# Kernel tuning notes

Hardware: AMD Instinct MI355X
Metric: run time of the kernel (lower is better)

The kernel has to match this reference:

```python
import jax, jax.numpy as jnp
import numpy as np

IN_F, OUT_F = 256, 256
GRID, ORDER = 5, 3
K = GRID + ORDER + 1  # 9 knots
EPS_MINMAX = 1e-7     # K.epsilon()
EPS_BN = 1e-3         # keras BatchNormalization default epsilon


def setup_inputs() -> dict:
    key = jax.random.key(0)
    ks = jax.random.split(key, 4)
    x = jax.random.normal(ks[0], (32, 32, 32, IN_F), dtype=jnp.float32)
    he = lambda k, shape, fan_in: jax.random.normal(k, shape, jnp.float32) * np.sqrt(2.0 / fan_in)
    base_weight = he(ks[1], (IN_F, OUT_F), IN_F)
    spline_weight = he(ks[2], (OUT_F, IN_F, K), IN_F * K)
    spline_scaler = jnp.ones((OUT_F, IN_F), jnp.float32)
    return {
        'x': x,
        'base_weight': base_weight,
        'spline_weight': spline_weight,
        'spline_scaler': spline_scaler,
        'bn_base_gamma': jnp.ones((OUT_F,), jnp.float32),
        'bn_base_beta': jnp.zeros((OUT_F,), jnp.float32),
        'bn_base_mean': jnp.zeros((OUT_F,), jnp.float32),
        'bn_base_var': jnp.ones((OUT_F,), jnp.float32),
        'bn_spline_gamma': jnp.ones((OUT_F,), jnp.float32),
        'bn_spline_beta': jnp.zeros((OUT_F,), jnp.float32),
        'bn_spline_mean': jnp.zeros((OUT_F,), jnp.float32),
        'bn_spline_var': jnp.ones((OUT_F,), jnp.float32),
    }


def _bn(z, gamma, beta, mean, var):
    # Keras BatchNormalization, inference mode (training=False)
    return gamma * (z - mean) * jax.lax.rsqrt(var + EPS_BN) + beta


def reference(x, base_weight, spline_weight, spline_scaler,
              bn_base_gamma, bn_base_beta, bn_base_mean, bn_base_var,
              bn_spline_gamma, bn_spline_beta, bn_spline_mean, bn_spline_var):
    B, H, W, _ = x.shape
    xf = x.reshape(-1, IN_F)  # [N, in]

    # base path: GEMM -> BN -> SiLU
    base = xf @ base_weight
    base = jax.nn.silu(_bn(base, bn_base_gamma, bn_base_beta, bn_base_mean, bn_base_var))

    # min-max normalize per feature over the flattened batch
    x_min = jnp.min(xf, axis=0, keepdims=True)
    x_max = jnp.max(xf, axis=0, keepdims=True)
    xn = (xf - x_min) / (x_max - x_min + EPS_MINMAX)

    # triangle basis: relu(1 - |x - knot|), knots = linspace(-1, 1, K)
    knots = jnp.linspace(-1.0, 1.0, K, dtype=jnp.float32)
    basis = jnp.maximum(0.0, 1.0 - jnp.abs(xn[:, :, None] - knots[None, None, :]))  # [N, in, K]

    # scaled spline weight, flattened GEMM
    w = (spline_weight * spline_scaler[:, :, None]).reshape(OUT_F, IN_F * K)  # [out, in*K]
    spline = basis.reshape(-1, IN_F * K) @ w.T  # [N, out]
    spline = _bn(spline, bn_spline_gamma, bn_spline_beta, bn_spline_mean, bn_spline_var)

    out = base + spline
    return out.reshape(B, H, W, OUT_F)
```

## Files before the change

kernel.cpp:

```cpp
#include <hip/hip_runtime.h>
#include <stdint.h>
#include <stddef.h>

typedef _Float16 h2 __attribute__((ext_vector_type(2)));
typedef _Float16 h8 __attribute__((ext_vector_type(8)));
typedef float f4 __attribute__((ext_vector_type(4)));

union Hfrag { h2 p[4]; h8 v; };

#define WS_PMIN   0
#define WS_PMAX   524288
#define WS_BT     0
#define WS_SMALL  1048576
#define WS_SCALEV (WS_SMALL + 0)
#define WS_BKN    (WS_SMALL + 1024)
#define WS_C0     (WS_SMALL + 3072)
#define WS_BSC    (WS_SMALL + 4096)
#define WS_BSH    (WS_SMALL + 5120)
#define WS_SSC    (WS_SMALL + 6144)
#define WS_SSH    (WS_SMALL + 7168)

__global__ __launch_bounds__(256) void kan_minmax(const float* __restrict__ x,
                                                  float* __restrict__ pmin,
                                                  float* __restrict__ pmax) {
  __shared__ f4 smn[4][64], smx[4][64];
  const int b = blockIdx.x, t = threadIdx.x;
  const int fq = t & 63, rg = t >> 6;
  const float* p = x + (size_t)b * 64 * 256 + (size_t)rg * 16 * 256 + fq * 4;
  f4 mn = (f4)(3.402823466e38f), mx = (f4)(-3.402823466e38f);
#pragma unroll
  for (int j = 0; j < 16; ++j) {
    f4 v = *(const f4*)(p + (size_t)j * 256);
    mn = __builtin_elementwise_min(mn, v);
    mx = __builtin_elementwise_max(mx, v);
  }
  smn[rg][fq] = mn; smx[rg][fq] = mx;
  __syncthreads();
  if (rg == 0) {
#pragma unroll
    for (int g = 1; g < 4; ++g) {
      mn = __builtin_elementwise_min(mn, smn[g][fq]);
      mx = __builtin_elementwise_max(mx, smx[g][fq]);
    }
    *(f4*)(pmin + (size_t)b * 256 + fq * 4) = mn;
    *(f4*)(pmax + (size_t)b * 256 + fq * 4) = mx;
  }
}

__global__ __launch_bounds__(256) void kan_finalize(
    const float* __restrict__ pmin, const float* __restrict__ pmax,
    const float* __restrict__ g1, const float* __restrict__ b1,
    const float* __restrict__ m1, const float* __restrict__ v1,
    const float* __restrict__ g2, const float* __restrict__ b2,
    const float* __restrict__ m2, const float* __restrict__ v2,
    float* __restrict__ scalev, _Float16* __restrict__ bkn,
    float* __restrict__ bscv, float* __restrict__ bshv,
    float* __restrict__ sscv, float* __restrict__ sshv) {
  __shared__ float smn[4][64], smx[4][64];
  const int t = threadIdx.x;
  const int ol = t & 63, pg = t >> 6;
  const int o = blockIdx.x * 64 + ol;
  float mn = 3.402823466e38f, mx = -3.402823466e38f;
  for (int p = pg * 128; p < pg * 128 + 128; ++p) {
    mn = fminf(mn, pmin[(size_t)p * 256 + o]);
    mx = fmaxf(mx, pmax[(size_t)p * 256 + o]);
  }
  smn[pg][ol] = mn; smx[pg][ol] = mx;
  __syncthreads();
  if (pg == 0) {
#pragma unroll
    for (int g = 1; g < 4; ++g) {
      mn = fminf(mn, smn[g][ol]);
      mx = fmaxf(mx, smx[g][ol]);
    }
    const float rng = mx - mn + 1e-7f;
    scalev[o] = 1.0f / rng;
    const float step = 0.25f * rng;
#pragma unroll
    for (int j = 0; j < 4; ++j)
      bkn[j * 256 + o] = (_Float16)(mn + step * (float)j);
    const float bs = g1[o] / sqrtf(v1[o] + 1e-3f);
    bscv[o] = bs;
    bshv[o] = b1[o] - m1[o] * bs;
    const float ss = g2[o] / sqrtf(v2[o] + 1e-3f);
    sscv[o] = ss;
    sshv[o] = b2[o] - m2[o] * ss;
  }
}

__global__ __launch_bounds__(256) void kan_buildw(
    const float* __restrict__ spline_w, const float* __restrict__ spline_s,
    const float* __restrict__ base_w, const float* __restrict__ scalev,
    _Float16* __restrict__ Bt, float* __restrict__ C0) {
  const int og = blockIdx.x;
  const int i  = threadIdx.x;
  const float* wp = spline_w + (size_t)(og * 256 + i) * 9;
  const float w1 = wp[1], w2 = wp[2], w3 = wp[3], w4 = wp[4];
  const float w5 = wp[5], w6 = wp[6], w7 = wp[7], w8 = wp[8];
  const float s  = spline_s[og * 256 + i];
  const float sc = scalev[i];
  const float wp0 = 0.25f*w1 + 0.5f*w2 + 0.75f*w3 + w4 + 0.75f*w5 + 0.5f*w6 + 0.25f*w7;
  float wj[4];
  wj[0] = (w5 + w6 + w7 + w8) - (w1 + w2 + w3 + w4);
  wj[1] = w1 - 2.0f * w5;
  wj[2] = w2 - 2.0f * w6;
  wj[3] = w3 - 2.0f * w7;
  const float ssc = s * sc;
  const int half = og >> 7, o = og & 127, ic = i >> 5, kk = i & 31;
#pragma unroll
  for (int j = 0; j < 4; ++j) {
    const int ks = j * 8 + ic;
    Bt[((size_t)(ks * 2 + half) * 128 + o) * 32 + kk] = (_Float16)(wj[j] * ssc);
  }
  Bt[((size_t)((32 + ic) * 2 + half) * 128 + o) * 32 + kk] =
      (_Float16)base_w[(size_t)i * 256 + og];
  __shared__ float red[256];
  red[i] = wp0 * s;
  __syncthreads();
  for (int st = 128; st > 0; st >>= 1) {
    if (i < st) red[i] += red[i + st];
    __syncthreads();
  }
  if (i == 0) C0[og] = red[0];
}

__global__ __launch_bounds__(256, 2) void kan_gemm(
    const float* __restrict__ x, const _Float16* __restrict__ Bt,
    const _Float16* __restrict__ bkn, const float* __restrict__ C0,
    const float* __restrict__ bscv, const float* __restrict__ bshv,
    const float* __restrict__ sscv, const float* __restrict__ sshv,
    float* __restrict__ out) {
  const int tid = threadIdx.x;
  const int lane = tid & 63;
  const int wv = tid >> 6;
  const int wm = wv >> 1, wn = wv & 1;
  const int lr = lane & 15, lg = lane >> 4;
  const int mt = blockIdx.x & 255, nt = blockIdx.x >> 8;

  const int rowA = mt * 128 + wm * 64 + lr;
  const int colB = wn * 64 + lr;

  f4 accS[4][4], accB[4][4];
#pragma unroll
  for (int m = 0; m < 4; ++m)
#pragma unroll
    for (int n = 0; n < 4; ++n) { accS[m][n] = (f4)0.0f; accB[m][n] = (f4)0.0f; }

  const char* btbase = (const char*)Bt + (size_t)nt * 8192 + (size_t)colB * 64 + (size_t)lg * 16;

  h2 hz; hz[0] = (_Float16)0.0f; hz[1] = (_Float16)0.0f;

  f4 xa[4], xb[4];
  {
    const int ib = lg * 8;
#pragma unroll
    for (int m = 0; m < 4; ++m) {
      const float* px = x + (size_t)(rowA + m * 16) * 256 + ib;
      xa[m] = *(const f4*)px; xb[m] = *(const f4*)(px + 4);
    }
  }

#pragma unroll 1
  for (int ic = 0; ic < 8; ++ic) {
    Hfrag bb[4];
#pragma unroll
    for (int j = 0; j < 4; ++j)
      bb[j].v = *(const h8*)(bkn + j * 256 + ic * 32 + lg * 8);

    Hfrag xh[4];
#pragma unroll
    for (int m = 0; m < 4; ++m) {
      xh[m].p[0][0] = (_Float16)xa[m].x; xh[m].p[0][1] = (_Float16)xa[m].y;
      xh[m].p[1][0] = (_Float16)xa[m].z; xh[m].p[1][1] = (_Float16)xa[m].w;
      xh[m].p[2][0] = (_Float16)xb[m].x; xh[m].p[2][1] = (_Float16)xb[m].y;
      xh[m].p[3][0] = (_Float16)xb[m].z; xh[m].p[3][1] = (_Float16)xb[m].w;
    }

    if (ic < 7) {
      const int ib = (ic + 1) * 32 + lg * 8;
#pragma unroll
      for (int m = 0; m < 4; ++m) {
        const float* px = x + (size_t)(rowA + m * 16) * 256 + ib;
        xa[m] = *(const f4*)px; xb[m] = *(const f4*)(px + 4);
      }
    }

    const char* bpic = btbase + (size_t)ic * 16384;

#pragma unroll
    for (int it = 0; it < 4; ++it) {
      Hfrag bf[4];
#pragma unroll
      for (int n = 0; n < 4; ++n)
        bf[n].v = *(const h8*)(bpic + (size_t)it * 131072 + n * 1024);
      Hfrag af[4];
#pragma unroll
      for (int m = 0; m < 4; ++m)
#pragma unroll
        for (int q = 0; q < 4; ++q) {
          h2 d = xh[m].p[q] - bb[it].p[q];
          af[m].p[q] = __builtin_elementwise_max(d, hz);
        }
#pragma unroll
      for (int m = 0; m < 4; ++m)
#pragma unroll
        for (int n = 0; n < 4; ++n)
          accS[m][n] = __builtin_amdgcn_mfma_f32_16x16x32_f16(af[m].v, bf[n].v, accS[m][n], 0, 0, 0);
    }

    {
      Hfrag bf[4];
#pragma unroll
      for (int n = 0; n < 4; ++n)
        bf[n].v = *(const h8*)(bpic + 524288 + n * 1024);
#pragma unroll
      for (int m = 0; m < 4; ++m)
#pragma unroll
        for (int n = 0; n < 4; ++n)
          accB[m][n] = __builtin_amdgcn_mfma_f32_16x16x32_f16(xh[m].v, bf[n].v, accB[m][n], 0, 0, 0);
    }
  }

#pragma unroll
  for (int n = 0; n < 4; ++n) {
    const int col = nt * 128 + colB + n * 16;
    const float vbs = bscv[col], vbh = bshv[col];
    const float vss = sscv[col];
    const float vsh = sshv[col] + vss * C0[col];
#pragma unroll
    for (int m = 0; m < 4; ++m) {
      const int row0 = mt * 128 + wm * 64 + m * 16 + lg * 4;
#pragma unroll
      for (int r = 0; r < 4; ++r) {
        const float zb = accB[m][n][r] * vbs + vbh;
        const float si = zb / (1.0f + __expf(-zb));
        const float val = si + accS[m][n][r] * vss + vsh;
        out[(size_t)(row0 + r) * 256 + col] = val;
      }
    }
  }
}

extern "C" void kernel_launch(void* const* d_in, const int* in_sizes, int n_in,
                              void* d_out, int out_size, void* d_ws, size_t ws_size,
                              hipStream_t stream) {
  const float* x        = (const float*)d_in[0];
  const float* base_w   = (const float*)d_in[1];
  const float* spline_w = (const float*)d_in[2];
  const float* spline_s = (const float*)d_in[3];
  const float* g1 = (const float*)d_in[4];
  const float* b1 = (const float*)d_in[5];
  const float* m1 = (const float*)d_in[6];
  const float* v1 = (const float*)d_in[7];
  const float* g2 = (const float*)d_in[8];
  const float* b2 = (const float*)d_in[9];
  const float* m2 = (const float*)d_in[10];
  const float* v2 = (const float*)d_in[11];
  float* out = (float*)d_out;
  char* ws = (char*)d_ws;

  float* pmin     = (float*)(ws + WS_PMIN);
  float* pmax     = (float*)(ws + WS_PMAX);
  _Float16* Bt    = (_Float16*)(ws + WS_BT);
  float* scalev   = (float*)(ws + WS_SCALEV);
  _Float16* bkn   = (_Float16*)(ws + WS_BKN);
  float* C0       = (float*)(ws + WS_C0);
  float* bscv     = (float*)(ws + WS_BSC);
  float* bshv     = (float*)(ws + WS_BSH);
  float* sscv     = (float*)(ws + WS_SSC);
  float* sshv     = (float*)(ws + WS_SSH);

  kan_minmax<<<512, 256, 0, stream>>>(x, pmin, pmax);
  kan_finalize<<<4, 256, 0, stream>>>(pmin, pmax, g1, b1, m1, v1, g2, b2, m2, v2,
                                      scalev, bkn, bscv, bshv, sscv, sshv);
  kan_buildw<<<256, 256, 0, stream>>>(spline_w, spline_s, base_w, scalev, Bt, C0);
  kan_gemm<<<512, 256, 0, stream>>>(x, Bt, bkn, C0, bscv, bshv, sscv, sshv, out);
}
```

Measured before the change: 155.0 us.

## Parallelize min/max finalize over 64 blocks and double-buffer B fragments in GEMM

The finalize kernel now runs as 64 blocks that each reduce 4 features across all 512 partials with vector loads and a shared-memory tree, replacing 4 blocks that looped serially over partials. In the GEMM main loop, B fragments are double-buffered so the next spline tile's loads are issued before the current tile's MFMAs. Knot fragments are loaded per step instead of all at once, and the prefetch of the next x chunk moves behind a sched_barrier. The aim is to cut the serial latency of the small finalize kernel and hide global-load latency in the GEMM, at the cost of more live registers.

```diff
diff --git a/kernel.cpp b/kernel.cpp
--- a/kernel.cpp
+++ b/kernel.cpp
@@ -56,35 +56,40 @@
     float* __restrict__ scalev, _Float16* __restrict__ bkn,
     float* __restrict__ bscv, float* __restrict__ bshv,
     float* __restrict__ sscv, float* __restrict__ sshv) {
-  __shared__ float smn[4][64], smx[4][64];
-  const int t = threadIdx.x;
-  const int ol = t & 63, pg = t >> 6;
-  const int o = blockIdx.x * 64 + ol;
-  float mn = 3.402823466e38f, mx = -3.402823466e38f;
-  for (int p = pg * 128; p < pg * 128 + 128; ++p) {
-    mn = fminf(mn, pmin[(size_t)p * 256 + o]);
-    mx = fmaxf(mx, pmax[(size_t)p * 256 + o]);
-  }
-  smn[pg][ol] = mn; smx[pg][ol] = mx;
+  __shared__ f4 smn[256], smx[256];
+  const int t = threadIdx.x, q = blockIdx.x;
+  const float* pm = pmin + (size_t)t * 256 + q * 4;
+  const float* px = pmax + (size_t)t * 256 + q * 4;
+  f4 mn = __builtin_elementwise_min(*(const f4*)pm, *(const f4*)(pm + 256 * 256));
+  f4 mx = __builtin_elementwise_max(*(const f4*)px, *(const f4*)(px + 256 * 256));
+  smn[t] = mn; smx[t] = mx;
   __syncthreads();
-  if (pg == 0) {
-#pragma unroll
-    for (int g = 1; g < 4; ++g) {
-      mn = fminf(mn, smn[g][ol]);
-      mx = fmaxf(mx, smx[g][ol]);
-    }
-    const float rng = mx - mn + 1e-7f;
-    scalev[o] = 1.0f / rng;
-    const float step = 0.25f * rng;
-#pragma unroll
-    for (int j = 0; j < 4; ++j)
-      bkn[j * 256 + o] = (_Float16)(mn + step * (float)j);
-    const float bs = g1[o] / sqrtf(v1[o] + 1e-3f);
-    bscv[o] = bs;
-    bshv[o] = b1[o] - m1[o] * bs;
-    const float ss = g2[o] / sqrtf(v2[o] + 1e-3f);
-    sscv[o] = ss;
-    sshv[o] = b2[o] - m2[o] * ss;
+  for (int st = 128; st > 0; st >>= 1) {
+    if (t < st) {
+      smn[t] = __builtin_elementwise_min(smn[t], smn[t + st]);
+      smx[t] = __builtin_elementwise_max(smx[t], smx[t + st]);
+    }
+    __syncthreads();
+  }
+  if (t == 0) {
+    const f4 fmn = smn[0], fmx = smx[0];
+#pragma unroll
+    for (int j = 0; j < 4; ++j) {
+      const int o = q * 4 + j;
+      const float mnS = fmn[j], mxS = fmx[j];
+      const float rng = mxS - mnS + 1e-7f;
+      scalev[o] = 1.0f / rng;
+      const float step = 0.25f * rng;
+#pragma unroll
+      for (int jj = 0; jj < 4; ++jj)
+        bkn[jj * 256 + o] = (_Float16)(mnS + step * (float)jj);
+      const float bs = g1[o] / sqrtf(v1[o] + 1e-3f);
+      bscv[o] = bs;
+      bshv[o] = b1[o] - m1[o] * bs;
+      const float ss = g2[o] / sqrtf(v2[o] + 1e-3f);
+      sscv[o] = ss;
+      sshv[o] = b2[o] - m2[o] * ss;
+    }
   }
 }
 
@@ -160,12 +165,36 @@
     }
   }
 
+#define SPLINE_STEP(J, BF)                                                   \
+  {                                                                          \
+    Hfrag bbj;                                                               \
+    bbj.v = *(const h8*)(bkn + (J) * 256 + ic * 32 + lg * 8);                \
+    _Pragma("unroll")                                                        \
+    for (int m = 0; m < 4; ++m) {                                            \
+      Hfrag afm;                                                             \
+      _Pragma("unroll")                                                      \
+      for (int qq = 0; qq < 4; ++qq) {                                       \
+        h2 d = xh[m].p[qq] - bbj.p[qq];                                      \
+        afm.p[qq] = __builtin_elementwise_max(d, hz);                        \
+      }                                                                      \
+      _Pragma("unroll")                                                      \
+      for (int n = 0; n < 4; ++n)                                            \
+        accS[m][n] = __builtin_amdgcn_mfma_f32_16x16x32_f16(afm.v, BF[n].v,  \
+                                                            accS[m][n], 0, 0, 0); \
+    }                                                                        \
+  }
+
+#define LOADB(BF, BYTEOFF)                                                   \
+  _Pragma("unroll")                                                          \
+  for (int n = 0; n < 4; ++n)                                                \
+    BF[n].v = *(const h8*)(bpic + (BYTEOFF) + n * 1024);
+
 #pragma unroll 1
   for (int ic = 0; ic < 8; ++ic) {
-    Hfrag bb[4];
-#pragma unroll
-    for (int j = 0; j < 4; ++j)
-      bb[j].v = *(const h8*)(bkn + j * 256 + ic * 32 + lg * 8);
+    const char* bpic = btbase + (size_t)ic * 16384;
+
+    Hfrag bfA[4], bfB[4];
+    LOADB(bfA, 0)
 
     Hfrag xh[4];
 #pragma unroll
@@ -176,6 +205,22 @@
       xh[m].p[3][0] = (_Float16)xb[m].z; xh[m].p[3][1] = (_Float16)xb[m].w;
     }
 
+    LOADB(bfB, 131072)
+    SPLINE_STEP(0, bfA)
+    LOADB(bfA, 262144)
+    SPLINE_STEP(1, bfB)
+    LOADB(bfB, 393216)
+    SPLINE_STEP(2, bfA)
+    LOADB(bfA, 524288)
+    SPLINE_STEP(3, bfB)
+
+#pragma unroll
+    for (int m = 0; m < 4; ++m)
+#pragma unroll
+      for (int n = 0; n < 4; ++n)
+        accB[m][n] = __builtin_amdgcn_mfma_f32_16x16x32_f16(xh[m].v, bfA[n].v, accB[m][n], 0, 0, 0);
+
+    __builtin_amdgcn_sched_barrier(0);
     if (ic < 7) {
       const int ib = (ic + 1) * 32 + lg * 8;
 #pragma unroll
@@ -184,42 +229,9 @@
         xa[m] = *(const f4*)px; xb[m] = *(const f4*)(px + 4);
       }
     }
-
-    const char* bpic = btbase + (size_t)ic * 16384;
-
-#pragma unroll
-    for (int it = 0; it < 4; ++it) {
-      Hfrag bf[4];
-#pragma unroll
-      for (int n = 0; n < 4; ++n)
-        bf[n].v = *(const h8*)(bpic + (size_t)it * 131072 + n * 1024);
-      Hfrag af[4];
-#pragma unroll
-      for (int m = 0; m < 4; ++m)
-#pragma unroll
-        for (int q = 0; q < 4; ++q) {
-          h2 d = xh[m].p[q] - bb[it].p[q];
-          af[m].p[q] = __builtin_elementwise_max(d, hz);
-        }
-#pragma unroll
-      for (int m = 0; m < 4; ++m)
-#pragma unroll
-        for (int n = 0; n < 4; ++n)
-          accS[m][n] = __builtin_amdgcn_mfma_f32_16x16x32_f16(af[m].v, bf[n].v, accS[m][n], 0, 0, 0);
-    }
-
-    {
-      Hfrag bf[4];
-#pragma unroll
-      for (int n = 0; n < 4; ++n)
-        bf[n].v = *(const h8*)(bpic + 524288 + n * 1024);
-#pragma unroll
-      for (int m = 0; m < 4; ++m)
-#pragma unroll
-        for (int n = 0; n < 4; ++n)
-          accB[m][n] = __builtin_amdgcn_mfma_f32_16x16x32_f16(xh[m].v, bf[n].v, accB[m][n], 0, 0, 0);
-    }
-  }
+  }
+#undef SPLINE_STEP
+#undef LOADB
 
 #pragma unroll
   for (int n = 0; n < 4; ++n) {
@@ -271,8 +283,8 @@
   float* sshv     = (float*)(ws + WS_SSH);
 
   kan_minmax<<<512, 256, 0, stream>>>(x, pmin, pmax);
-  kan_finalize<<<4, 256, 0, stream>>>(pmin, pmax, g1, b1, m1, v1, g2, b2, m2, v2,
-                                      scalev, bkn, bscv, bshv, sscv, sshv);
+  kan_finalize<<<64, 256, 0, stream>>>(pmin, pmax, g1, b1, m1, v1, g2, b2, m2, v2,
+                                       scalev, bkn, bscv, bshv, sscv, sshv);
   kan_buildw<<<256, 256, 0, stream>>>(spline_w, spline_s, base_w, scalev, Bt, C0);
   kan_gemm<<<512, 256, 0, stream>>>(x, Bt, bkn, C0, bscv, bshv, sscv, sshv, out);
 }
```

After: 151.2 us. -2.5%, faster.
